# Performance work log

Hardware: AMD Instinct MI355X
Metric: run time of the kernel (lower is better)

The kernel has to match this reference:

```python
import jax, jax.numpy as jnp
import numpy as np
from jax import lax

# Shared Conv2d [1,1] + BN + ReLU is represented as a per-point affine (BN folded
# into conv weight/bias at eval) followed by ReLU, matching inference-mode math.

B, N1, N2, K = 8, 8192, 2048, 8
C1, C2 = 64, 128
MLP0, MLP1, MLP2 = 128, 128, 128  # mlp=[128,128], mlp2=[128]


def setup_inputs() -> dict:
    key = jax.random.key(0)
    ks = jax.random.split(key, 10)
    sc = lambda fan_in: 1.0 / np.sqrt(fan_in)
    return {
        "xyz1": jax.random.normal(ks[0], (B, N1, 3), jnp.float32),
        "xyz2": jax.random.normal(ks[1], (B, N2, 3), jnp.float32),
        "feat1": jax.random.normal(ks[2], (B, N1, C1), jnp.float32),
        "feat2": jax.random.normal(ks[3], (B, N2, C2), jnp.float32),
        "W0": jax.random.normal(ks[4], (C2 + 3, MLP0), jnp.float32) * sc(C2 + 3),
        "b0": jnp.zeros((MLP0,), jnp.float32),
        "W1": jax.random.normal(ks[5], (MLP0, MLP1), jnp.float32) * sc(MLP0),
        "b1": jnp.zeros((MLP1,), jnp.float32),
        "W2": jax.random.normal(ks[6], (MLP1 + C1, MLP2), jnp.float32) * sc(MLP1 + C1),
        "b2": jnp.zeros((MLP2,), jnp.float32),
    }


def _knn_idx(xyz1, xyz2, k):
    # squared distances (B, N1, N2); top-k nearest in xyz2 for each xyz1 point
    d2 = jnp.sum((xyz1[:, :, None, :] - xyz2[:, None, :, :]) ** 2, axis=-1)
    _, idx = lax.top_k(-d2, k)  # (B, N1, K)
    return idx


def _gather(src, idx):
    # src: (B, N2, C), idx: (B, N1, K) -> (B, N1, K, C)
    return jax.vmap(lambda s, i: s[i])(src, idx)


def reference(xyz1, xyz2, feat1, feat2, W0, b0, W1, b1, W2, b2):
    idx = _knn_idx(xyz1, xyz2, K)
    xyz2_g = _gather(xyz2, idx)            # (B, N1, K, 3)
    feat2_g = _gather(feat2, idx)          # (B, N1, K, C2)
    xyz_diff = xyz2_g - xyz1[:, :, None, :]
    net = jnp.concatenate([feat2_g, xyz_diff], axis=-1)  # (B, N1, K, C2+3)
    net = jax.nn.relu(net @ W0 + b0)
    net = jax.nn.relu(net @ W1 + b1)       # (B, N1, K, MLP1)
    pooled = jnp.max(net, axis=2)          # max pooling over neighbors
    cat = jnp.concatenate([pooled, feat1], axis=-1)      # (B, N1, MLP1+C1)
    out = jax.nn.relu(cat @ W2 + b2)       # (B, N1, MLP2)
    return out
```

## Files before the change

kernel.cpp:

```cpp
#include <hip/hip_runtime.h>
#include <hip/hip_bf16.h>

constexpr int B_  = 8;
constexpr int N1_ = 8192;
constexpr int N2_ = 2048;
constexpr int K_  = 8;

typedef short bf16x8 __attribute__((ext_vector_type(8)));
typedef float f32x4  __attribute__((ext_vector_type(4)));

__device__ __forceinline__ short f2b(float x) {
    __hip_bfloat16 h = __float2bfloat16(x);
    return *reinterpret_cast<short*>(&h);
}

__global__ __launch_bounds__(256) void prep_feat2(const float* __restrict__ feat2,
                                                  short* __restrict__ feat2b) {
    const int i = blockIdx.x * 256 + threadIdx.x;
    const float4 v = ((const float4*)feat2)[i];
    uint2 o;
    o.x = (unsigned short)f2b(v.x) | ((unsigned)(unsigned short)f2b(v.y) << 16);
    o.y = (unsigned short)f2b(v.z) | ((unsigned)(unsigned short)f2b(v.w) << 16);
    ((uint2*)feat2b)[i] = o;
}

__global__ __launch_bounds__(256) void prep_weights(
    const float* __restrict__ W0, const float* __restrict__ W1,
    const float* __restrict__ W2, const float* __restrict__ xyz2,
    short* __restrict__ W0T, short* __restrict__ W1T, short* __restrict__ W2T,
    float4* __restrict__ xpack) {
    int i = blockIdx.x * 256 + threadIdx.x;
    if (i < 128 * 160) {
        const int n = i / 160, k = i % 160;
        W0T[i] = (k < 131) ? f2b(W0[k * 128 + n]) : (short)0;
        return;
    }
    i -= 128 * 160;
    if (i < 128 * 128) {
        const int n = i >> 7, k = i & 127;
        W1T[i] = f2b(W1[k * 128 + n]);
        return;
    }
    i -= 128 * 128;
    if (i < 128 * 192) {
        const int n = i / 192, k = i % 192;
        W2T[i] = f2b(W2[k * 128 + n]);
        return;
    }
    i -= 128 * 192;
    xpack[i] = make_float4(xyz2[i * 3 + 0], xyz2[i * 3 + 1], xyz2[i * 3 + 2], 0.f);
}

constexpr int LCAP = 76;

__global__ __launch_bounds__(256) void knn_list(const float* __restrict__ xyz1,
                                                const float4* __restrict__ xpack,
                                                int* __restrict__ idx) {
    __shared__ __align__(16) unsigned short sMem[256 * 78];
    float* sD = (float*)sMem;
    int*   sI = (int*)sMem + 64 * 33;

    const int b = blockIdx.y;
    const int lane = threadIdx.x & 63;
    const int s = threadIdx.x >> 6;
    const int tid = threadIdx.x;
    const int n = blockIdx.x * 64 + lane;

    const float* q = xyz1 + ((size_t)b * N1_ + n) * 3;
    const float qx = q[0], qy = q[1], qz = q[2];
    const float4* P = xpack + (size_t)b * N2_ + s * 512;

    unsigned bd[K_];
#pragma unroll
    for (int t = 0; t < K_; ++t) bd[t] = __float_as_uint(3.0e38f);
    int cnt = 0;

    for (int j0 = 0; j0 < 512; j0 += 8) {
        float d2[8];
#pragma unroll
        for (int u = 0; u < 8; ++u) {
#pragma clang fp contract(off)
            const float4 p = P[j0 + u];
            const float dx = qx - p.x;
            const float dy = qy - p.y;
            const float dz = qz - p.z;
            const float dx2 = dx * dx;
            const float dy2 = dy * dy;
            const float dz2 = dz * dz;
            d2[u] = (dx2 + dy2) + dz2;
        }
#pragma unroll
        for (int u = 0; u < 8; ++u) {
            const unsigned xu = __float_as_uint(d2[u]);
            const bool acc = xu < bd[K_ - 1];
            const int slot = acc ? (cnt < LCAP ? cnt : LCAP) : LCAP + 1;
            sMem[tid * 78 + slot] = (unsigned short)(j0 + u);
            cnt += acc ? 1 : 0;
            bd[K_ - 1] = bd[K_ - 1] < xu ? bd[K_ - 1] : xu;
#pragma unroll
            for (int t = K_ - 1; t >= 1; --t) {
                const unsigned lo = bd[t - 1] < bd[t] ? bd[t - 1] : bd[t];
                const unsigned hi = bd[t - 1] < bd[t] ? bd[t] : bd[t - 1];
                bd[t - 1] = lo; bd[t] = hi;
            }
        }
    }

    float rd[K_];
    int   ri[K_];
#pragma unroll
    for (int t = 0; t < K_; ++t) { rd[t] = 3.0e38f; ri[t] = 0; }
    const int m = cnt < LCAP ? cnt : LCAP;
    for (int t = 0;; ++t) {
        const bool act = t < m;
        if (!__any(act)) break;
        if (act) {
#pragma clang fp contract(off)
            const int jl = sMem[tid * 78 + t];
            const float4 p = P[jl];
            const float dx = qx - p.x;
            const float dy = qy - p.y;
            const float dz = qz - p.z;
            const float dx2 = dx * dx;
            const float dy2 = dy * dy;
            const float dz2 = dz * dz;
            const float d2 = (dx2 + dy2) + dz2;
            if (d2 < rd[K_ - 1]) {
                rd[K_ - 1] = d2; ri[K_ - 1] = s * 512 + jl;
#pragma unroll
                for (int t2 = K_ - 1; t2 >= 1; --t2) {
                    if (rd[t2] < rd[t2 - 1]) {
                        float td = rd[t2]; rd[t2] = rd[t2 - 1]; rd[t2 - 1] = td;
                        int   ti = ri[t2]; ri[t2] = ri[t2 - 1]; ri[t2 - 1] = ti;
                    }
                }
            }
        }
    }

    if (__any(cnt > LCAP)) {
        if (cnt > LCAP) {
#pragma unroll
            for (int t = 0; t < K_; ++t) { rd[t] = 3.0e38f; ri[t] = 0; }
            for (int j = 0; j < 512; ++j) {
#pragma clang fp contract(off)
                const float4 p = P[j];
                const float dx = qx - p.x;
                const float dy = qy - p.y;
                const float dz = qz - p.z;
                const float dx2 = dx * dx;
                const float dy2 = dy * dy;
                const float dz2 = dz * dz;
                const float d2 = (dx2 + dy2) + dz2;
                if (d2 < rd[K_ - 1]) {
                    rd[K_ - 1] = d2; ri[K_ - 1] = s * 512 + j;
#pragma unroll
                    for (int t2 = K_ - 1; t2 >= 1; --t2) {
                        if (rd[t2] < rd[t2 - 1]) {
                            float td = rd[t2]; rd[t2] = rd[t2 - 1]; rd[t2 - 1] = td;
                            int   ti = ri[t2]; ri[t2] = ri[t2 - 1]; ri[t2 - 1] = ti;
                        }
                    }
                }
            }
        }
    }

    __syncthreads();
#pragma unroll
    for (int t = 0; t < K_; ++t) {
        sD[lane * 33 + s * 8 + t] = rd[t];
        sI[lane * 33 + s * 8 + t] = ri[t];
    }
    __syncthreads();

    if (tid < 64) {
        const int qq = tid;
        int h[4] = {0, 0, 0, 0};
        const int base = (b * N1_ + n) * K_;
#pragma unroll
        for (int t = 0; t < K_; ++t) {
            float best = 3.1e38f;
            int   bidx = 0, bs = 0;
#pragma unroll
            for (int ss = 0; ss < 4; ++ss) {
                if (h[ss] < 8) {
                    const float d = sD[qq * 33 + ss * 8 + h[ss]];
                    if (d < best) { best = d; bidx = sI[qq * 33 + ss * 8 + h[ss]]; bs = ss; }
                }
            }
            h[bs]++;
            idx[base + t] = bidx;
        }
    }
}

__global__ __launch_bounds__(256) void fused_mfma(
    const float* __restrict__ xyz1, const float* __restrict__ xyz2,
    const float* __restrict__ feat1,
    const float* __restrict__ b0, const float* __restrict__ b1,
    const float* __restrict__ b2,
    const short* __restrict__ feat2b, const short* __restrict__ W0T,
    const short* __restrict__ W1T, const short* __restrict__ W2T,
    const int* __restrict__ idx, float* __restrict__ out) {
    __shared__ __align__(16) short sA1[128 * 136];
    __shared__ __align__(16) short sCat[16 * 200];

    const int b = blockIdx.y;
    const int n0 = blockIdx.x * 16;
    const int tid = threadIdx.x;
    const int wave = tid >> 6, lane = tid & 63;
    const int q = lane >> 4, l15 = lane & 15;
    const int mBase = (wave & 1) * 64, nBase = (wave >> 1) * 64;

#pragma unroll
    for (int u = 0; u < 4; ++u) {
        const int e = tid * 4 + u;
        const int p = e >> 6, c = e & 63;
        sCat[p * 200 + 128 + c] = f2b(feat1[((size_t)b * N1_ + n0 + p) * 64 + c]);
    }

    int jrow[4];
#pragma unroll
    for (int mt = 0; mt < 4; ++mt) {
        const int row = mBase + mt * 16 + l15;
        const int p = row >> 3, kk = row & 7;
        jrow[mt] = idx[((size_t)b * N1_ + (n0 + p)) * K_ + kk];
    }

    bf16x8 a4[4];
#pragma unroll
    for (int mt = 0; mt < 4; ++mt) {
        bf16x8 v = {0, 0, 0, 0, 0, 0, 0, 0};
        if (q == 0) {
            const int row = mBase + mt * 16 + l15;
            const int p = row >> 3;
            const int n = n0 + p;
            const int j = jrow[mt];
            const float dx = xyz2[((size_t)b * N2_ + j) * 3 + 0] - xyz1[((size_t)b * N1_ + n) * 3 + 0];
            const float dy = xyz2[((size_t)b * N2_ + j) * 3 + 1] - xyz1[((size_t)b * N1_ + n) * 3 + 1];
            const float dz = xyz2[((size_t)b * N2_ + j) * 3 + 2] - xyz1[((size_t)b * N1_ + n) * 3 + 2];
            v[0] = f2b(dx); v[1] = f2b(dy); v[2] = f2b(dz);
        }
        a4[mt] = v;
    }

    const f32x4 zero4 = {0.f, 0.f, 0.f, 0.f};

    f32x4 acc[4][4];
#pragma unroll
    for (int mt = 0; mt < 4; ++mt)
#pragma unroll
        for (int nt = 0; nt < 4; ++nt) acc[mt][nt] = zero4;

#pragma unroll
    for (int ks = 0; ks < 4; ++ks) {
        bf16x8 af[4], bf[4];
#pragma unroll
        for (int mt = 0; mt < 4; ++mt)
            af[mt] = *(const bf16x8*)(feat2b + ((size_t)b * N2_ + jrow[mt]) * 128 + ks * 32 + q * 8);
#pragma unroll
        for (int nt = 0; nt < 4; ++nt)
            bf[nt] = *(const bf16x8*)(W0T + (nBase + nt * 16 + l15) * 160 + ks * 32 + q * 8);
#pragma unroll
        for (int mt = 0; mt < 4; ++mt)
#pragma unroll
            for (int nt = 0; nt < 4; ++nt)
                acc[mt][nt] = __builtin_amdgcn_mfma_f32_16x16x32_bf16(af[mt], bf[nt], acc[mt][nt], 0, 0, 0);
    }
    {
        bf16x8 bf[4];
#pragma unroll
        for (int nt = 0; nt < 4; ++nt)
            bf[nt] = *(const bf16x8*)(W0T + (nBase + nt * 16 + l15) * 160 + 128 + q * 8);
#pragma unroll
        for (int mt = 0; mt < 4; ++mt)
#pragma unroll
            for (int nt = 0; nt < 4; ++nt)
                acc[mt][nt] = __builtin_amdgcn_mfma_f32_16x16x32_bf16(a4[mt], bf[nt], acc[mt][nt], 0, 0, 0);
    }

    float b0v[4];
#pragma unroll
    for (int nt = 0; nt < 4; ++nt) b0v[nt] = b0[nBase + nt * 16 + l15];
#pragma unroll
    for (int mt = 0; mt < 4; ++mt)
#pragma unroll
        for (int nt = 0; nt < 4; ++nt)
#pragma unroll
            for (int r = 0; r < 4; ++r) {
                const int row = mBase + mt * 16 + q * 4 + r;
                const int col = nBase + nt * 16 + l15;
                sA1[row * 136 + col] = f2b(fmaxf(acc[mt][nt][r] + b0v[nt], 0.0f));
            }
    __syncthreads();

    f32x4 acc2[4][4];
#pragma unroll
    for (int mt = 0; mt < 4; ++mt)
#pragma unroll
        for (int nt = 0; nt < 4; ++nt) acc2[mt][nt] = zero4;

#pragma unroll
    for (int ks = 0; ks < 4; ++ks) {
        bf16x8 af[4], bf[4];
#pragma unroll
        for (int mt = 0; mt < 4; ++mt)
            af[mt] = *(const bf16x8*)(sA1 + (mBase + mt * 16 + l15) * 136 + ks * 32 + q * 8);
#pragma unroll
        for (int nt = 0; nt < 4; ++nt)
            bf[nt] = *(const bf16x8*)(W1T + (nBase + nt * 16 + l15) * 128 + ks * 32 + q * 8);
#pragma unroll
        for (int mt = 0; mt < 4; ++mt)
#pragma unroll
            for (int nt = 0; nt < 4; ++nt)
                acc2[mt][nt] = __builtin_amdgcn_mfma_f32_16x16x32_bf16(af[mt], bf[nt], acc2[mt][nt], 0, 0, 0);
    }

    float b1v[4];
#pragma unroll
    for (int nt = 0; nt < 4; ++nt) b1v[nt] = b1[nBase + nt * 16 + l15];
#pragma unroll
    for (int mt = 0; mt < 4; ++mt)
#pragma unroll
        for (int nt = 0; nt < 4; ++nt) {
            float vm = fmaxf(acc2[mt][nt][0] + b1v[nt], 0.0f);
#pragma unroll
            for (int r = 1; r < 4; ++r) vm = fmaxf(vm, acc2[mt][nt][r] + b1v[nt]);
            const float other = __shfl_xor(vm, 16);
            const float pool = fmaxf(vm, other);
            if ((q & 1) == 0) {
                const int pp = (mBase >> 3) + mt * 2 + (q >> 1);
                sCat[pp * 200 + nBase + nt * 16 + l15] = f2b(pool);
            }
        }
    __syncthreads();

    f32x4 acc3[2];
    acc3[0] = zero4; acc3[1] = zero4;
    const int nB2 = wave * 32;
#pragma unroll
    for (int ks = 0; ks < 6; ++ks) {
        const bf16x8 a2 = *(const bf16x8*)(sCat + l15 * 200 + ks * 32 + q * 8);
#pragma unroll
        for (int nt = 0; nt < 2; ++nt) {
            const bf16x8 b2f = *(const bf16x8*)(W2T + (nB2 + nt * 16 + l15) * 192 + ks * 32 + q * 8);
            acc3[nt] = __builtin_amdgcn_mfma_f32_16x16x32_bf16(a2, b2f, acc3[nt], 0, 0, 0);
        }
    }
    float b2v[2];
#pragma unroll
    for (int nt = 0; nt < 2; ++nt) b2v[nt] = b2[nB2 + nt * 16 + l15];
#pragma unroll
    for (int nt = 0; nt < 2; ++nt)
#pragma unroll
        for (int r = 0; r < 4; ++r) {
            const int p = q * 4 + r;
            const int col = nB2 + nt * 16 + l15;
            out[((size_t)(b * N1_ + n0 + p)) * 128 + col] = fmaxf(acc3[nt][r] + b2v[nt], 0.0f);
        }
}

extern "C" void kernel_launch(void* const* d_in, const int* in_sizes, int n_in,
                              void* d_out, int out_size, void* d_ws, size_t ws_size,
                              hipStream_t stream) {
    const float* xyz1  = (const float*)d_in[0];
    const float* xyz2  = (const float*)d_in[1];
    const float* feat1 = (const float*)d_in[2];
    const float* feat2 = (const float*)d_in[3];
    const float* W0    = (const float*)d_in[4];
    const float* b0    = (const float*)d_in[5];
    const float* W1    = (const float*)d_in[6];
    const float* b1    = (const float*)d_in[7];
    const float* W2    = (const float*)d_in[8];
    const float* b2    = (const float*)d_in[9];
    float* out = (float*)d_out;

    char* ws = (char*)d_ws;
    int*    idx    = (int*)(ws + 0);
    short*  feat2b = (short*)(ws + 2097152);
    short*  W0T    = (short*)(ws + 6291456);
    short*  W1T    = (short*)(ws + 6332416);
    short*  W2T    = (short*)(ws + 6365184);
    float4* xpack  = (float4*)(ws + 6414336);

    prep_feat2<<<2048, 256, 0, stream>>>(feat2, feat2b);
    prep_weights<<<304, 256, 0, stream>>>(W0, W1, W2, xyz2, W0T, W1T, W2T, xpack);
    knn_list<<<dim3(N1_ / 64, B_), 256, 0, stream>>>(xyz1, xpack, idx);
    fused_mfma<<<dim3(N1_ / 16, B_), 256, 0, stream>>>(xyz1, xyz2, feat1, b0, b1, b2,
                                                       feat2b, W0T, W1T, W2T, idx, out);
}
```

Before: 359.1 us.

## Batch KNN threshold updates with sorting networks and stage gathered features in LDS

The KNN scan now compares each group of 8 candidates against a fixed threshold. It then merges them into the running top-8 with a bitonic-style sorting network instead of a per-candidate insertion chain, and the candidate list in shared memory is transposed to a slot-major layout. The fused MLP kernel now cooperatively gathers the neighbour feature rows and xyz differences into a padded LDS tile before the first GEMM. This replaces per-wave scattered global loads and folds the xyz term into a fifth K-step. The changes add a barrier, reuse the LDS buffer for the first-layer output, and drop unrolling on some loops.

```diff
diff --git a/kernel.cpp b/kernel.cpp
--- a/kernel.cpp
+++ b/kernel.cpp
@@ -13,6 +13,10 @@
     __hip_bfloat16 h = __float2bfloat16(x);
     return *reinterpret_cast<short*>(&h);
 }
+
+#define CASU(a, b) { const unsigned _lo = (a) < (b) ? (a) : (b); \
+                     const unsigned _hi = (a) < (b) ? (b) : (a); \
+                     (a) = _lo; (b) = _hi; }
 
 __global__ __launch_bounds__(256) void prep_feat2(const float* __restrict__ feat2,
                                                   short* __restrict__ feat2b) {
@@ -53,10 +57,10 @@
 
 constexpr int LCAP = 76;
 
-__global__ __launch_bounds__(256) void knn_list(const float* __restrict__ xyz1,
+__global__ __launch_bounds__(256) void knn_lazy(const float* __restrict__ xyz1,
                                                 const float4* __restrict__ xpack,
                                                 int* __restrict__ idx) {
-    __shared__ __align__(16) unsigned short sMem[256 * 78];
+    __shared__ __align__(16) unsigned short sMem[78 * 256];
     float* sD = (float*)sMem;
     int*   sI = (int*)sMem + 64 * 33;
 
@@ -76,7 +80,7 @@
     int cnt = 0;
 
     for (int j0 = 0; j0 < 512; j0 += 8) {
-        float d2[8];
+        unsigned xu[8];
 #pragma unroll
         for (int u = 0; u < 8; ++u) {
 #pragma clang fp contract(off)
@@ -87,23 +91,37 @@
             const float dx2 = dx * dx;
             const float dy2 = dy * dy;
             const float dz2 = dz * dz;
-            d2[u] = (dx2 + dy2) + dz2;
-        }
+            xu[u] = __float_as_uint((dx2 + dy2) + dz2);
+        }
+        const unsigned thr = bd[K_ - 1];
 #pragma unroll
         for (int u = 0; u < 8; ++u) {
-            const unsigned xu = __float_as_uint(d2[u]);
-            const bool acc = xu < bd[K_ - 1];
-            const int slot = acc ? (cnt < LCAP ? cnt : LCAP) : LCAP + 1;
-            sMem[tid * 78 + slot] = (unsigned short)(j0 + u);
+            const bool acc = xu[u] < thr;
+            const int capped = cnt < LCAP ? cnt : LCAP;
+            const int slot = acc ? capped : (LCAP + 1);
+            sMem[slot * 256 + tid] = (unsigned short)(j0 + u);
             cnt += acc ? 1 : 0;
-            bd[K_ - 1] = bd[K_ - 1] < xu ? bd[K_ - 1] : xu;
-#pragma unroll
-            for (int t = K_ - 1; t >= 1; --t) {
-                const unsigned lo = bd[t - 1] < bd[t] ? bd[t - 1] : bd[t];
-                const unsigned hi = bd[t - 1] < bd[t] ? bd[t] : bd[t - 1];
-                bd[t - 1] = lo; bd[t] = hi;
-            }
-        }
+        }
+        CASU(xu[0], xu[1]); CASU(xu[2], xu[3]); CASU(xu[4], xu[5]); CASU(xu[6], xu[7]);
+        CASU(xu[0], xu[2]); CASU(xu[1], xu[3]); CASU(xu[4], xu[6]); CASU(xu[5], xu[7]);
+        CASU(xu[1], xu[2]); CASU(xu[5], xu[6]); CASU(xu[0], xu[4]); CASU(xu[3], xu[7]);
+        CASU(xu[1], xu[5]); CASU(xu[2], xu[6]);
+        CASU(xu[1], xu[4]); CASU(xu[3], xu[6]);
+        CASU(xu[2], xu[4]); CASU(xu[3], xu[5]);
+        CASU(xu[3], xu[4]);
+        unsigned t0 = bd[0] < xu[7] ? bd[0] : xu[7];
+        unsigned t1 = bd[1] < xu[6] ? bd[1] : xu[6];
+        unsigned t2 = bd[2] < xu[5] ? bd[2] : xu[5];
+        unsigned t3 = bd[3] < xu[4] ? bd[3] : xu[4];
+        unsigned t4 = bd[4] < xu[3] ? bd[4] : xu[3];
+        unsigned t5 = bd[5] < xu[2] ? bd[5] : xu[2];
+        unsigned t6 = bd[6] < xu[1] ? bd[6] : xu[1];
+        unsigned t7 = bd[7] < xu[0] ? bd[7] : xu[0];
+        CASU(t0, t4); CASU(t1, t5); CASU(t2, t6); CASU(t3, t7);
+        CASU(t0, t2); CASU(t1, t3); CASU(t4, t6); CASU(t5, t7);
+        CASU(t0, t1); CASU(t2, t3); CASU(t4, t5); CASU(t6, t7);
+        bd[0] = t0; bd[1] = t1; bd[2] = t2; bd[3] = t3;
+        bd[4] = t4; bd[5] = t5; bd[6] = t6; bd[7] = t7;
     }
 
     float rd[K_];
@@ -116,7 +134,7 @@
         if (!__any(act)) break;
         if (act) {
 #pragma clang fp contract(off)
-            const int jl = sMem[tid * 78 + t];
+            const int jl = sMem[t * 256 + tid];
             const float4 p = P[jl];
             const float dx = qx - p.x;
             const float dy = qy - p.y;
@@ -203,48 +221,52 @@
     const short* __restrict__ feat2b, const short* __restrict__ W0T,
     const short* __restrict__ W1T, const short* __restrict__ W2T,
     const int* __restrict__ idx, float* __restrict__ out) {
-    __shared__ __align__(16) short sA1[128 * 136];
+    __shared__ __align__(16) short sA[128 * 168];
     __shared__ __align__(16) short sCat[16 * 200];
 
     const int b = blockIdx.y;
     const int n0 = blockIdx.x * 16;
     const int tid = threadIdx.x;
+
+    {
+        const int row = tid >> 1, half = tid & 1;
+        const int p = row >> 3, kk = row & 7;
+        const int n = n0 + p;
+        const int j = idx[((size_t)b * N1_ + n) * K_ + kk];
+        const uint4* src = (const uint4*)(feat2b + ((size_t)(b * N2_ + j)) * 128 + half * 64);
+        uint4* dst = (uint4*)(sA + row * 168 + half * 64);
+#pragma unroll
+        for (int t = 0; t < 8; ++t) dst[t] = src[t];
+        uint4* pad = (uint4*)(sA + row * 168 + 128 + half * 16);
+        if (half == 0) {
+            const float dx = xyz2[((size_t)b * N2_ + j) * 3 + 0] - xyz1[((size_t)b * N1_ + n) * 3 + 0];
+            const float dy = xyz2[((size_t)b * N2_ + j) * 3 + 1] - xyz1[((size_t)b * N1_ + n) * 3 + 1];
+            const float dz = xyz2[((size_t)b * N2_ + j) * 3 + 2] - xyz1[((size_t)b * N1_ + n) * 3 + 2];
+            uint4 v;
+            v.x = (unsigned short)f2b(dx) | ((unsigned)(unsigned short)f2b(dy) << 16);
+            v.y = (unsigned short)f2b(dz);
+            v.z = 0; v.w = 0;
+            pad[0] = v;
+            pad[1] = make_uint4(0, 0, 0, 0);
+        } else {
+            pad[0] = make_uint4(0, 0, 0, 0);
+            pad[1] = make_uint4(0, 0, 0, 0);
+        }
+    }
+    {
+#pragma unroll
+        for (int u = 0; u < 4; ++u) {
+            const int e = tid * 4 + u;
+            const int p = e >> 6, c = e & 63;
+            sCat[p * 200 + 128 + c] = f2b(feat1[((size_t)b * N1_ + n0 + p) * 64 + c]);
+        }
+    }
+    __syncthreads();
+
     const int wave = tid >> 6, lane = tid & 63;
     const int q = lane >> 4, l15 = lane & 15;
     const int mBase = (wave & 1) * 64, nBase = (wave >> 1) * 64;
 
-#pragma unroll
-    for (int u = 0; u < 4; ++u) {
-        const int e = tid * 4 + u;
-        const int p = e >> 6, c = e & 63;
-        sCat[p * 200 + 128 + c] = f2b(feat1[((size_t)b * N1_ + n0 + p) * 64 + c]);
-    }
-
-    int jrow[4];
-#pragma unroll
-    for (int mt = 0; mt < 4; ++mt) {
-        const int row = mBase + mt * 16 + l15;
-        const int p = row >> 3, kk = row & 7;
-        jrow[mt] = idx[((size_t)b * N1_ + (n0 + p)) * K_ + kk];
-    }
-
-    bf16x8 a4[4];
-#pragma unroll
-    for (int mt = 0; mt < 4; ++mt) {
-        bf16x8 v = {0, 0, 0, 0, 0, 0, 0, 0};
-        if (q == 0) {
-            const int row = mBase + mt * 16 + l15;
-            const int p = row >> 3;
-            const int n = n0 + p;
-            const int j = jrow[mt];
-            const float dx = xyz2[((size_t)b * N2_ + j) * 3 + 0] - xyz1[((size_t)b * N1_ + n) * 3 + 0];
-            const float dy = xyz2[((size_t)b * N2_ + j) * 3 + 1] - xyz1[((size_t)b * N1_ + n) * 3 + 1];
-            const float dz = xyz2[((size_t)b * N2_ + j) * 3 + 2] - xyz1[((size_t)b * N1_ + n) * 3 + 2];
-            v[0] = f2b(dx); v[1] = f2b(dy); v[2] = f2b(dz);
-        }
-        a4[mt] = v;
-    }
-
     const f32x4 zero4 = {0.f, 0.f, 0.f, 0.f};
 
     f32x4 acc[4][4];
@@ -253,12 +275,11 @@
 #pragma unroll
         for (int nt = 0; nt < 4; ++nt) acc[mt][nt] = zero4;
 
-#pragma unroll
-    for (int ks = 0; ks < 4; ++ks) {
+    for (int ks = 0; ks < 5; ++ks) {
         bf16x8 af[4], bf[4];
 #pragma unroll
         for (int mt = 0; mt < 4; ++mt)
-            af[mt] = *(const bf16x8*)(feat2b + ((size_t)b * N2_ + jrow[mt]) * 128 + ks * 32 + q * 8);
+            af[mt] = *(const bf16x8*)(sA + (mBase + mt * 16 + l15) * 168 + ks * 32 + q * 8);
 #pragma unroll
         for (int nt = 0; nt < 4; ++nt)
             bf[nt] = *(const bf16x8*)(W0T + (nBase + nt * 16 + l15) * 160 + ks * 32 + q * 8);
@@ -268,21 +289,11 @@
             for (int nt = 0; nt < 4; ++nt)
                 acc[mt][nt] = __builtin_amdgcn_mfma_f32_16x16x32_bf16(af[mt], bf[nt], acc[mt][nt], 0, 0, 0);
     }
-    {
-        bf16x8 bf[4];
-#pragma unroll
-        for (int nt = 0; nt < 4; ++nt)
-            bf[nt] = *(const bf16x8*)(W0T + (nBase + nt * 16 + l15) * 160 + 128 + q * 8);
-#pragma unroll
-        for (int mt = 0; mt < 4; ++mt)
-#pragma unroll
-            for (int nt = 0; nt < 4; ++nt)
-                acc[mt][nt] = __builtin_amdgcn_mfma_f32_16x16x32_bf16(a4[mt], bf[nt], acc[mt][nt], 0, 0, 0);
-    }
 
     float b0v[4];
 #pragma unroll
     for (int nt = 0; nt < 4; ++nt) b0v[nt] = b0[nBase + nt * 16 + l15];
+    __syncthreads();
 #pragma unroll
     for (int mt = 0; mt < 4; ++mt)
 #pragma unroll
@@ -291,7 +302,7 @@
             for (int r = 0; r < 4; ++r) {
                 const int row = mBase + mt * 16 + q * 4 + r;
                 const int col = nBase + nt * 16 + l15;
-                sA1[row * 136 + col] = f2b(fmaxf(acc[mt][nt][r] + b0v[nt], 0.0f));
+                sA[row * 136 + col] = f2b(fmaxf(acc[mt][nt][r] + b0v[nt], 0.0f));
             }
     __syncthreads();
 
@@ -301,12 +312,11 @@
 #pragma unroll
         for (int nt = 0; nt < 4; ++nt) acc2[mt][nt] = zero4;
 
-#pragma unroll
     for (int ks = 0; ks < 4; ++ks) {
         bf16x8 af[4], bf[4];
 #pragma unroll
         for (int mt = 0; mt < 4; ++mt)
-            af[mt] = *(const bf16x8*)(sA1 + (mBase + mt * 16 + l15) * 136 + ks * 32 + q * 8);
+            af[mt] = *(const bf16x8*)(sA + (mBase + mt * 16 + l15) * 136 + ks * 32 + q * 8);
 #pragma unroll
         for (int nt = 0; nt < 4; ++nt)
             bf[nt] = *(const bf16x8*)(W1T + (nBase + nt * 16 + l15) * 128 + ks * 32 + q * 8);
@@ -339,7 +349,6 @@
     f32x4 acc3[2];
     acc3[0] = zero4; acc3[1] = zero4;
     const int nB2 = wave * 32;
-#pragma unroll
     for (int ks = 0; ks < 6; ++ks) {
         const bf16x8 a2 = *(const bf16x8*)(sCat + l15 * 200 + ks * 32 + q * 8);
 #pragma unroll
@@ -386,7 +395,7 @@
 
     prep_feat2<<<2048, 256, 0, stream>>>(feat2, feat2b);
     prep_weights<<<304, 256, 0, stream>>>(W0, W1, W2, xyz2, W0T, W1T, W2T, xpack);
-    knn_list<<<dim3(N1_ / 64, B_), 256, 0, stream>>>(xyz1, xpack, idx);
+    knn_lazy<<<dim3(N1_ / 64, B_), 256, 0, stream>>>(xyz1, xpack, idx);
     fused_mfma<<<dim3(N1_ / 16, B_), 256, 0, stream>>>(xyz1, xyz2, feat1, b0, b1, b2,
                                                        feat2b, W0T, W1T, W2T, idx, out);
 }
```

New measurement: 326.0 us. -9.2%, faster.
